# Kernel tuning notes

Hardware: AMD Instinct MI355X
Metric: run time of the kernel (lower is better)

Reference implementation:

```python
import jax, jax.numpy as jnp
import numpy as np

B, S, D = 2, 2048, 640
H, DH = 8, 80  # heads, dim_head
SCALE = DH ** -0.5


def setup_inputs() -> dict:
    key = jax.random.key(0)
    ks = jax.random.split(key, 7)
    std = D ** -0.5
    return {
        "x": jax.random.normal(ks[0], (B, S, D), jnp.float32),
        "encoder_hidden_states": jax.random.normal(ks[1], (B, S, D), jnp.float32),
        # Linear weights stored as [in, out] so application is x @ W
        "Wq": jax.random.normal(ks[2], (D, H * DH), jnp.float32) * std,
        "Wk": jax.random.normal(ks[3], (D, H * DH), jnp.float32) * std,
        "Wv": jax.random.normal(ks[4], (D, H * DH), jnp.float32) * std,
        "Wo": jax.random.normal(ks[5], (H * DH, D), jnp.float32) * std,
        "bo": jax.random.normal(ks[6], (D,), jnp.float32) * 0.01,
    }


def reference(x, encoder_hidden_states, Wq, Wk, Wv, Wo, bo):
    # projections (to_q/to_k/to_v have bias=False)
    q = x @ Wq                      # [B, S, H*DH]
    k = encoder_hidden_states @ Wk  # [B, S, H*DH]
    v = encoder_hidden_states @ Wv  # [B, S, H*DH]

    def split_heads(t):
        b, s, _ = t.shape
        return t.reshape(b, s, H, DH).transpose(0, 2, 1, 3)  # [B, H, S, DH]

    q, k, v = split_heads(q), split_heads(k), split_heads(v)

    # the torch loop over bh-chunks computes plain softmax attention; same math fused
    scores = jnp.einsum("bhid,bhjd->bhij", q, k) * SCALE  # [B, H, Sq, Skv]
    attn = jax.nn.softmax(scores, axis=-1)
    out = jnp.einsum("bhij,bhjd->bhid", attn, v)          # [B, H, Sq, DH]

    out = out.transpose(0, 2, 1, 3).reshape(x.shape[0], x.shape[1], H * DH)
    return out @ Wo + bo  # to_out[0]; Dropout(p=0) is identity
```

## Files before the change

### kernel.cpp

```cpp
#include <hip/hip_runtime.h>
#include <hip/hip_bf16.h>

typedef __bf16 v4bf __attribute__((ext_vector_type(4)));
typedef __bf16 v8bf __attribute__((ext_vector_type(8)));
typedef float  v4f  __attribute__((ext_vector_type(4)));

namespace {
constexpr int Bb  = 2;
constexpr int Ss  = 2048;
constexpr int Dd  = 640;
constexpr int Hh  = 8;
constexpr int DHh = 80;
constexpr int Mm  = Bb * Ss;
constexpr float kQScale = 0.11180339887498949f * 1.4426950408889634f;

__device__ __forceinline__ float4 ld4(const float* p) {
  return *reinterpret_cast<const float4*>(p);
}
}

__global__ __launch_bounds__(256)
void wtrans_kernel(const float* __restrict__ Wq, const float* __restrict__ Wk,
                   const float* __restrict__ Wv, const float* __restrict__ Wo,
                   __bf16* __restrict__ Wtq, __bf16* __restrict__ Wtk,
                   __bf16* __restrict__ Wtv, __bf16* __restrict__ Wto) {
  const int z = blockIdx.z;
  const float* W = (z == 0) ? Wq : (z == 1) ? Wk : (z == 2) ? Wv : Wo;
  __bf16* Wt = (z == 0) ? Wtq : (z == 1) ? Wtk : (z == 2) ? Wtv : Wto;
  const int k0 = blockIdx.y * 32, n0 = blockIdx.x * 32;
  __shared__ float t[32][33];
  const int tid = threadIdx.x;
  {
    int kr = tid >> 3, c4 = (tid & 7) * 4;
    float4 f = ld4(W + (size_t)(k0 + kr) * Dd + n0 + c4);
    t[kr][c4 + 0] = f.x; t[kr][c4 + 1] = f.y;
    t[kr][c4 + 2] = f.z; t[kr][c4 + 3] = f.w;
  }
  __syncthreads();
  {
    int nr = tid >> 3, kc = (tid & 7) * 4;
    v4bf p;
#pragma unroll
    for (int u = 0; u < 4; ++u) p[u] = (__bf16)t[kc + u][nr];
    *reinterpret_cast<v4bf*>(&Wt[(size_t)(n0 + nr) * Dd + k0 + kc]) = p;
  }
}

template <bool AF32>
__device__ __forceinline__ void gemm_core_db(const void* __restrict__ Ap,
                                             const __bf16* __restrict__ Bt,
                                             __bf16* As, __bf16* Bs, int m0,
                                             int n0, int rh, int ch,
                                             v4f acc[4][4]) {
  constexpr int BUF = 128 * 40;
  constexpr int NKB = Dd / 32;
  const int tid = threadIdx.x;
  const int lane = tid & 63;
  const int quad = lane >> 4, l15 = lane & 15;
  const int lr = tid >> 1;
  const int lk = (tid & 1) * 16;
  const __bf16* Bg = Bt + (size_t)(n0 + lr) * Dd + lk;
  const float* Af = (const float*)Ap;
  const __bf16* Ab = (const __bf16*)Ap;

#pragma unroll
  for (int i = 0; i < 4; ++i)
#pragma unroll
    for (int j = 0; j < 4; ++j) acc[i][j] = (v4f){0.f, 0.f, 0.f, 0.f};

  v8bf a0, a1, b0, b1;
  if constexpr (AF32) {
    const float* ap = Af + (size_t)(m0 + lr) * Dd + lk;
    float4 f0 = ld4(ap), f1 = ld4(ap + 4), f2 = ld4(ap + 8), f3 = ld4(ap + 12);
    a0[0]=(__bf16)f0.x; a0[1]=(__bf16)f0.y; a0[2]=(__bf16)f0.z; a0[3]=(__bf16)f0.w;
    a0[4]=(__bf16)f1.x; a0[5]=(__bf16)f1.y; a0[6]=(__bf16)f1.z; a0[7]=(__bf16)f1.w;
    a1[0]=(__bf16)f2.x; a1[1]=(__bf16)f2.y; a1[2]=(__bf16)f2.z; a1[3]=(__bf16)f2.w;
    a1[4]=(__bf16)f3.x; a1[5]=(__bf16)f3.y; a1[6]=(__bf16)f3.z; a1[7]=(__bf16)f3.w;
  } else {
    const __bf16* ap = Ab + (size_t)(m0 + lr) * Dd + lk;
    a0 = *reinterpret_cast<const v8bf*>(ap);
    a1 = *reinterpret_cast<const v8bf*>(ap + 8);
  }
  b0 = *reinterpret_cast<const v8bf*>(Bg);
  b1 = *reinterpret_cast<const v8bf*>(Bg + 8);
  *reinterpret_cast<v8bf*>(&As[lr * 40 + lk])     = a0;
  *reinterpret_cast<v8bf*>(&As[lr * 40 + lk + 8]) = a1;
  *reinterpret_cast<v8bf*>(&Bs[lr * 40 + lk])     = b0;
  *reinterpret_cast<v8bf*>(&Bs[lr * 40 + lk + 8]) = b1;

  for (int it = 0; it < NKB; ++it) {
    if (it + 1 < NKB) {
      const int kb = (it + 1) * 32;
      if constexpr (AF32) {
        const float* ap = Af + (size_t)(m0 + lr) * Dd + kb + lk;
        float4 f0 = ld4(ap), f1 = ld4(ap + 4), f2 = ld4(ap + 8),
               f3 = ld4(ap + 12);
        a0[0]=(__bf16)f0.x; a0[1]=(__bf16)f0.y; a0[2]=(__bf16)f0.z; a0[3]=(__bf16)f0.w;
        a0[4]=(__bf16)f1.x; a0[5]=(__bf16)f1.y; a0[6]=(__bf16)f1.z; a0[7]=(__bf16)f1.w;
        a1[0]=(__bf16)f2.x; a1[1]=(__bf16)f2.y; a1[2]=(__bf16)f2.z; a1[3]=(__bf16)f2.w;
        a1[4]=(__bf16)f3.x; a1[5]=(__bf16)f3.y; a1[6]=(__bf16)f3.z; a1[7]=(__bf16)f3.w;
      } else {
        const __bf16* ap = Ab + (size_t)(m0 + lr) * Dd + kb + lk;
        a0 = *reinterpret_cast<const v8bf*>(ap);
        a1 = *reinterpret_cast<const v8bf*>(ap + 8);
      }
      b0 = *reinterpret_cast<const v8bf*>(Bg + kb);
      b1 = *reinterpret_cast<const v8bf*>(Bg + kb + 8);
    }
    __syncthreads();
    const int cur = (it & 1) * BUF, nxt = BUF - cur;
    v8bf af[4], bv[4];
#pragma unroll
    for (int i = 0; i < 4; ++i)
      af[i] = *reinterpret_cast<const v8bf*>(
          &As[cur + (rh + i * 16 + l15) * 40 + quad * 8]);
#pragma unroll
    for (int j = 0; j < 4; ++j)
      bv[j] = *reinterpret_cast<const v8bf*>(
          &Bs[cur + (ch + j * 16 + l15) * 40 + quad * 8]);
#pragma unroll
    for (int i = 0; i < 4; ++i)
#pragma unroll
      for (int j = 0; j < 4; ++j)
        acc[i][j] = __builtin_amdgcn_mfma_f32_16x16x32_bf16(af[i], bv[j],
                                                            acc[i][j], 0, 0, 0);
    if (it + 1 < NKB) {
      *reinterpret_cast<v8bf*>(&As[nxt + lr * 40 + lk])     = a0;
      *reinterpret_cast<v8bf*>(&As[nxt + lr * 40 + lk + 8]) = a1;
      *reinterpret_cast<v8bf*>(&Bs[nxt + lr * 40 + lk])     = b0;
      *reinterpret_cast<v8bf*>(&Bs[nxt + lr * 40 + lk + 8]) = b1;
    }
  }
}

__global__ __launch_bounds__(256)
void gemm_qkv_mfma(const float* __restrict__ x, const float* __restrict__ ehs,
                   const __bf16* __restrict__ Wtq,
                   const __bf16* __restrict__ Wtk,
                   const __bf16* __restrict__ Wtv, __bf16* __restrict__ qb,
                   __bf16* __restrict__ kbuf, __bf16* __restrict__ vb) {
  const int z = blockIdx.z;
  const float* A = (z == 0) ? x : ehs;
  const __bf16* Bt = (z == 0) ? Wtq : (z == 1) ? Wtk : Wtv;
  __bf16* C = (z == 0) ? qb : (z == 1) ? kbuf : vb;
  const float scale = (z == 0) ? kQScale : 1.0f;

  __shared__ __bf16 As[2 * 128 * 40];
  __shared__ __bf16 Bs[2 * 128 * 40];
  const int tid = threadIdx.x;
  const int w = tid >> 6, lane = tid & 63;
  const int quad = lane >> 4, l15 = lane & 15;
  const int m0 = blockIdx.y * 128, n0 = blockIdx.x * 128;
  const int rh = (w >> 1) * 64, ch = (w & 1) * 64;
  v4f acc[4][4];
  gemm_core_db<true>(A, Bt, As, Bs, m0, n0, rh, ch, acc);

  if (z == 2) {
#pragma unroll
    for (int i = 0; i < 4; ++i)
#pragma unroll
      for (int j = 0; j < 4; ++j) {
        int m = m0 + rh + i * 16 + quad * 4;
        int n = n0 + ch + j * 16 + l15;
        int bb = m >> 11, tok = m & 2047;
        v4bf pk;
#pragma unroll
        for (int r = 0; r < 4; ++r) pk[r] = (__bf16)acc[i][j][r];
        *reinterpret_cast<v4bf*>(&C[((size_t)bb * Dd + n) * Ss + tok]) = pk;
      }
  } else {
#pragma unroll
    for (int i = 0; i < 4; ++i)
#pragma unroll
      for (int j = 0; j < 4; ++j) {
        int m = m0 + rh + i * 16 + quad * 4;
        int n = n0 + ch + j * 16 + l15;
        int hh = n / DHh, d = n % DHh;
        int bb = m >> 11, tok = m & 2047;
        __bf16* base = &C[(((size_t)bb * Hh + hh) * Ss + tok) * DHh + d];
#pragma unroll
        for (int r = 0; r < 4; ++r)
          base[(size_t)r * DHh] = (__bf16)(acc[i][j][r] * scale);
      }
  }
}

__global__ __launch_bounds__(256)
void gemm_out_mfma(const __bf16* __restrict__ A, const __bf16* __restrict__ Bt,
                   const float* __restrict__ bias, float* __restrict__ out) {
  __shared__ __bf16 As[2 * 128 * 40];
  __shared__ __bf16 Bs[2 * 128 * 40];
  const int tid = threadIdx.x;
  const int w = tid >> 6, lane = tid & 63;
  const int quad = lane >> 4, l15 = lane & 15;
  const int m0 = blockIdx.y * 128, n0 = blockIdx.x * 128;
  const int rh = (w >> 1) * 64, ch = (w & 1) * 64;
  v4f acc[4][4];
  gemm_core_db<false>(A, Bt, As, Bs, m0, n0, rh, ch, acc);

#pragma unroll
  for (int i = 0; i < 4; ++i)
#pragma unroll
    for (int j = 0; j < 4; ++j) {
      int m = m0 + rh + i * 16 + quad * 4;
      int n = n0 + ch + j * 16 + l15;
      float bn = bias[n];
#pragma unroll
      for (int r = 0; r < 4; ++r)
        out[(size_t)(m + r) * Dd + n] = acc[i][j][r] + bn;
    }
}

__global__ __launch_bounds__(256, 2)
void attn_mfma_kernel(const __bf16* __restrict__ q,
                      const __bf16* __restrict__ k,
                      const __bf16* __restrict__ vtg, __bf16* __restrict__ o) {
  constexpr int QT = 64;
  constexpr int KT = 32;
  constexpr int KW = Ss / 4;
  constexpr int NIT = KW / KT;
  constexpr int LQ = 104;
  constexpr int LV = 40;
  constexpr int KS = KT * LQ;
  constexpr int VS = 96 * LV;
  constexpr int PS = QT * LV;
  constexpr int WSZ = KS + VS + PS;
  constexpr int LM = 100;

  __shared__ __align__(16) __bf16 smem[4 * WSZ];

  const int bh = blockIdx.x;
  const int b = bh >> 3, h = bh & 7;
  const int q0 = blockIdx.y * QT;
  const int tid = threadIdx.x;
  const int w = tid >> 6;
  const int lane = tid & 63;
  const int quad = lane >> 4;
  const int l15 = lane & 15;

  __bf16* ksw = smem + w * WSZ;
  __bf16* vtw = ksw + KS;
  __bf16* psw = vtw + VS;

  const __bf16* qg  = q + ((size_t)(b * Hh + h) * Ss + q0) * DHh;
  const __bf16* kgb = k + (size_t)(b * Hh + h) * Ss * DHh;
  const __bf16* vgb = vtg + ((size_t)b * Dd + h * DHh) * Ss;

  v8bf qf[4][3];
#pragma unroll
  for (int qt = 0; qt < 4; ++qt)
#pragma unroll
    for (int s = 0; s < 3; ++s) {
      if (s == 2 && quad >= 2) {
        qf[qt][s] = (v8bf){};
      } else {
        qf[qt][s] = *reinterpret_cast<const v8bf*>(
            qg + (size_t)(qt * 16 + l15) * DHh + s * 32 + quad * 8);
      }
    }

  int klr[5];
#pragma unroll
  for (int c = 0; c < 5; ++c) {
    int E = c * 512 + lane * 8;
    klr[c] = (E / DHh) * LQ + (E % DHh);
  }
  const int vgo = (lane >> 2) * Ss + (lane & 3) * 8;
  const int vlo = (lane >> 2) * LV + (lane & 3) * 8;

  {
    v8bf z8 = {};
    *reinterpret_cast<v8bf*>(&ksw[(lane >> 1) * LQ + 80 + (lane & 1) * 8]) = z8;
    v8bf pad = {};
    int vr = 80 + (lane >> 2);
    if (vr == 80) {
#pragma unroll
      for (int e = 0; e < 8; ++e) pad[e] = (__bf16)1.f;
    }
    *reinterpret_cast<v8bf*>(&vtw[vr * LV + (lane & 3) * 8]) = pad;
  }
  {
    const __bf16* kg = kgb + (size_t)(w * KW) * DHh;
#pragma unroll
    for (int c = 0; c < 5; ++c)
      *reinterpret_cast<v8bf*>(&ksw[klr[c]]) =
          *reinterpret_cast<const v8bf*>(kg + c * 512 + lane * 8);
  }

  v4f Oacc[4][6];
#pragma unroll
  for (int qt = 0; qt < 4; ++qt)
#pragma unroll
    for (int mt = 0; mt < 6; ++mt) Oacc[qt][mt] = (v4f){0.f, 0.f, 0.f, 0.f};

  for (int it = 0; it < NIT; ++it) {
    const bool pfK = (it + 1 < NIT);
    v8bf kreg[5];
    if (pfK) {
      const __bf16* kg = kgb + (size_t)(w * KW + (it + 1) * KT) * DHh;
#pragma unroll
      for (int c = 0; c < 5; ++c)
        kreg[c] = *reinterpret_cast<const v8bf*>(kg + c * 512 + lane * 8);
    }

    v4f sacc[4][2];
#pragma unroll
    for (int qt = 0; qt < 4; ++qt) {
      sacc[qt][0] = (v4f){0.f, 0.f, 0.f, 0.f};
      sacc[qt][1] = (v4f){0.f, 0.f, 0.f, 0.f};
    }
    __builtin_amdgcn_s_setprio(1);
#pragma unroll
    for (int s = 0; s < 3; ++s) {
      v8bf ak0 = *reinterpret_cast<const v8bf*>(
          &ksw[l15 * LQ + s * 32 + quad * 8]);
      v8bf ak1 = *reinterpret_cast<const v8bf*>(
          &ksw[(16 + l15) * LQ + s * 32 + quad * 8]);
#pragma unroll
      for (int qt = 0; qt < 4; ++qt) {
        sacc[qt][0] = __builtin_amdgcn_mfma_f32_16x16x32_bf16(
            ak0, qf[qt][s], sacc[qt][0], 0, 0, 0);
        sacc[qt][1] = __builtin_amdgcn_mfma_f32_16x16x32_bf16(
            ak1, qf[qt][s], sacc[qt][1], 0, 0, 0);
      }
    }

    v8bf vreg[5];
    {
      const __bf16* vg = vgb + (w * KW + it * KT);
#pragma unroll
      for (int c = 0; c < 5; ++c)
        vreg[c] = *reinterpret_cast<const v8bf*>(vg + vgo +
                                                 (size_t)c * 16 * Ss);
    }

    if (it > 0) {
      v8bf bp[4];
#pragma unroll
      for (int qt = 0; qt < 4; ++qt)
        bp[qt] = *reinterpret_cast<const v8bf*>(
            &psw[(qt * 16 + l15) * LV + quad * 8]);
#pragma unroll
      for (int mt = 0; mt < 6; ++mt) {
        v8bf av = *reinterpret_cast<const v8bf*>(
            &vtw[(mt * 16 + l15) * LV + quad * 8]);
#pragma unroll
        for (int qt = 0; qt < 4; ++qt)
          Oacc[qt][mt] = __builtin_amdgcn_mfma_f32_16x16x32_bf16(
              av, bp[qt], Oacc[qt][mt], 0, 0, 0);
      }
    }
    __builtin_amdgcn_s_setprio(0);

#pragma unroll
    for (int qt = 0; qt < 4; ++qt)
#pragma unroll
      for (int mt = 0; mt < 2; ++mt) {
        v4bf pk;
#pragma unroll
        for (int r = 0; r < 4; ++r) pk[r] = (__bf16)exp2f(sacc[qt][mt][r]);
        *reinterpret_cast<v4bf*>(
            &psw[(qt * 16 + l15) * LV + mt * 16 + quad * 4]) = pk;
      }

    if (pfK) {
#pragma unroll
      for (int c = 0; c < 5; ++c)
        *reinterpret_cast<v8bf*>(&ksw[klr[c]]) = kreg[c];
    }
#pragma unroll
    for (int c = 0; c < 5; ++c)
      *reinterpret_cast<v8bf*>(&vtw[vlo + c * 16 * LV]) = vreg[c];
  }

  {
    v8bf bp[4];
#pragma unroll
    for (int qt = 0; qt < 4; ++qt)
      bp[qt] = *reinterpret_cast<const v8bf*>(
          &psw[(qt * 16 + l15) * LV + quad * 8]);
    __builtin_amdgcn_s_setprio(1);
#pragma unroll
    for (int mt = 0; mt < 6; ++mt) {
      v8bf av = *reinterpret_cast<const v8bf*>(
          &vtw[(mt * 16 + l15) * LV + quad * 8]);
#pragma unroll
      for (int qt = 0; qt < 4; ++qt)
        Oacc[qt][mt] = __builtin_amdgcn_mfma_f32_16x16x32_bf16(
            av, bp[qt], Oacc[qt][mt], 0, 0, 0);
    }
    __builtin_amdgcn_s_setprio(0);
  }

  __syncthreads();
  float* mrg = (float*)smem;
  if (w >= 2) {
    float* base = mrg + (w - 2) * (QT * LM);
#pragma unroll
    for (int qt = 0; qt < 4; ++qt)
#pragma unroll
      for (int mt = 0; mt < 6; ++mt)
        *reinterpret_cast<v4f*>(
            &base[(qt * 16 + l15) * LM + mt * 16 + quad * 4]) = Oacc[qt][mt];
  }
  __syncthreads();
  if (w < 2) {
    const float* base = mrg + w * (QT * LM);
#pragma unroll
    for (int qt = 0; qt < 4; ++qt)
#pragma unroll
      for (int mt = 0; mt < 6; ++mt)
        Oacc[qt][mt] += *reinterpret_cast<const v4f*>(
            &base[(qt * 16 + l15) * LM + mt * 16 + quad * 4]);
  }
  __syncthreads();
  if (w == 1) {
#pragma unroll
    for (int qt = 0; qt < 4; ++qt)
#pragma unroll
      for (int mt = 0; mt < 6; ++mt)
        *reinterpret_cast<v4f*>(
            &mrg[(qt * 16 + l15) * LM + mt * 16 + quad * 4]) = Oacc[qt][mt];
  }
  __syncthreads();
  if (w == 0) {
#pragma unroll
    for (int qt = 0; qt < 4; ++qt)
#pragma unroll
      for (int mt = 0; mt < 6; ++mt)
        Oacc[qt][mt] += *reinterpret_cast<const v4f*>(
            &mrg[(qt * 16 + l15) * LM + mt * 16 + quad * 4]);
#pragma unroll
    for (int qt = 0; qt < 4; ++qt) {
      float lsum = __shfl(Oacc[qt][5][0], l15);
      float inv = 1.f / lsum;
      __bf16* og =
          o + (size_t)(b * Ss + q0 + qt * 16 + l15) * Dd + h * DHh;
#pragma unroll
      for (int mt = 0; mt < 5; ++mt) {
        v4bf pk;
#pragma unroll
        for (int r = 0; r < 4; ++r) pk[r] = (__bf16)(Oacc[qt][mt][r] * inv);
        *reinterpret_cast<v4bf*>(&og[mt * 16 + quad * 4]) = pk;
      }
    }
  }
}

extern "C" void kernel_launch(void* const* d_in, const int* in_sizes, int n_in,
                              void* d_out, int out_size, void* d_ws,
                              size_t ws_size, hipStream_t stream) {
  const float* x   = (const float*)d_in[0];
  const float* ehs = (const float*)d_in[1];
  const float* Wq  = (const float*)d_in[2];
  const float* Wk  = (const float*)d_in[3];
  const float* Wv  = (const float*)d_in[4];
  const float* Wo  = (const float*)d_in[5];
  const float* bo  = (const float*)d_in[6];
  float* out = (float*)d_out;

  __bf16* qb  = (__bf16*)d_ws;
  __bf16* kb  = qb + (size_t)Mm * Dd;
  __bf16* vb  = kb + (size_t)Mm * Dd;
  __bf16* ab  = vb + (size_t)Mm * Dd;
  __bf16* Wtq = ab + (size_t)Mm * Dd;
  __bf16* Wtk = Wtq + (size_t)Dd * Dd;
  __bf16* Wtv = Wtk + (size_t)Dd * Dd;
  __bf16* Wto = Wtv + (size_t)Dd * Dd;

  wtrans_kernel<<<dim3(Dd / 32, Dd / 32, 4), 256, 0, stream>>>(
      Wq, Wk, Wv, Wo, Wtq, Wtk, Wtv, Wto);
  gemm_qkv_mfma<<<dim3(Dd / 128, Mm / 128, 3), 256, 0, stream>>>(
      x, ehs, Wtq, Wtk, Wtv, qb, kb, vb);
  attn_mfma_kernel<<<dim3(Bb * Hh, Ss / 64), 256, 0, stream>>>(qb, kb, vb, ab);
  gemm_out_mfma<<<dim3(Dd / 128, Mm / 128), 256, 0, stream>>>(ab, Wto, bo,
                                                              out);
}
```

Measured before the change: 155.8 us.

## Fuse K and V projections sharing one A tile; use raw v_exp_f32 in attention

The QKV GEMM now launches two block types per output tile. One computes Q from x, the other computes both K and V from encoder_hidden_states. The second reuses a single loaded and bf16-converted A tile for two B matrices, which avoids reading and converting ehs twice. It doubles the accumulator registers (launch_bounds with 1 block), adds a third LDS buffer, and makes the two block types unbalanced in work. The attention softmax also replaces exp2f with the raw v_exp_f32 instruction, which skips the denormal and range handling.

```diff
diff --git a/kernel.cpp b/kernel.cpp
--- a/kernel.cpp
+++ b/kernel.cpp
@@ -16,6 +16,19 @@
 
 __device__ __forceinline__ float4 ld4(const float* p) {
   return *reinterpret_cast<const float4*>(p);
+}
+
+__device__ __forceinline__ v8bf pack8(float4 f0, float4 f1) {
+  v8bf p;
+  p[0]=(__bf16)f0.x; p[1]=(__bf16)f0.y; p[2]=(__bf16)f0.z; p[3]=(__bf16)f0.w;
+  p[4]=(__bf16)f1.x; p[5]=(__bf16)f1.y; p[6]=(__bf16)f1.z; p[7]=(__bf16)f1.w;
+  return p;
+}
+
+__device__ __forceinline__ float exp2_hw(float x) {
+  float r;
+  asm("v_exp_f32 %0, %1" : "=v"(r) : "v"(x));
+  return r;
 }
 }
 
@@ -71,11 +84,8 @@
   v8bf a0, a1, b0, b1;
   if constexpr (AF32) {
     const float* ap = Af + (size_t)(m0 + lr) * Dd + lk;
-    float4 f0 = ld4(ap), f1 = ld4(ap + 4), f2 = ld4(ap + 8), f3 = ld4(ap + 12);
-    a0[0]=(__bf16)f0.x; a0[1]=(__bf16)f0.y; a0[2]=(__bf16)f0.z; a0[3]=(__bf16)f0.w;
-    a0[4]=(__bf16)f1.x; a0[5]=(__bf16)f1.y; a0[6]=(__bf16)f1.z; a0[7]=(__bf16)f1.w;
-    a1[0]=(__bf16)f2.x; a1[1]=(__bf16)f2.y; a1[2]=(__bf16)f2.z; a1[3]=(__bf16)f2.w;
-    a1[4]=(__bf16)f3.x; a1[5]=(__bf16)f3.y; a1[6]=(__bf16)f3.z; a1[7]=(__bf16)f3.w;
+    a0 = pack8(ld4(ap), ld4(ap + 4));
+    a1 = pack8(ld4(ap + 8), ld4(ap + 12));
   } else {
     const __bf16* ap = Ab + (size_t)(m0 + lr) * Dd + lk;
     a0 = *reinterpret_cast<const v8bf*>(ap);
@@ -93,12 +103,8 @@
       const int kb = (it + 1) * 32;
       if constexpr (AF32) {
         const float* ap = Af + (size_t)(m0 + lr) * Dd + kb + lk;
-        float4 f0 = ld4(ap), f1 = ld4(ap + 4), f2 = ld4(ap + 8),
-               f3 = ld4(ap + 12);
-        a0[0]=(__bf16)f0.x; a0[1]=(__bf16)f0.y; a0[2]=(__bf16)f0.z; a0[3]=(__bf16)f0.w;
-        a0[4]=(__bf16)f1.x; a0[5]=(__bf16)f1.y; a0[6]=(__bf16)f1.z; a0[7]=(__bf16)f1.w;
-        a1[0]=(__bf16)f2.x; a1[1]=(__bf16)f2.y; a1[2]=(__bf16)f2.z; a1[3]=(__bf16)f2.w;
-        a1[4]=(__bf16)f3.x; a1[5]=(__bf16)f3.y; a1[6]=(__bf16)f3.z; a1[7]=(__bf16)f3.w;
+        a0 = pack8(ld4(ap), ld4(ap + 4));
+        a1 = pack8(ld4(ap + 8), ld4(ap + 12));
       } else {
         const __bf16* ap = Ab + (size_t)(m0 + lr) * Dd + kb + lk;
         a0 = *reinterpret_cast<const v8bf*>(ap);
@@ -133,29 +139,139 @@
   }
 }
 
-__global__ __launch_bounds__(256)
+__global__ __launch_bounds__(256, 1)
 void gemm_qkv_mfma(const float* __restrict__ x, const float* __restrict__ ehs,
                    const __bf16* __restrict__ Wtq,
                    const __bf16* __restrict__ Wtk,
                    const __bf16* __restrict__ Wtv, __bf16* __restrict__ qb,
                    __bf16* __restrict__ kbuf, __bf16* __restrict__ vb) {
-  const int z = blockIdx.z;
-  const float* A = (z == 0) ? x : ehs;
-  const __bf16* Bt = (z == 0) ? Wtq : (z == 1) ? Wtk : Wtv;
-  __bf16* C = (z == 0) ? qb : (z == 1) ? kbuf : vb;
-  const float scale = (z == 0) ? kQScale : 1.0f;
-
-  __shared__ __bf16 As[2 * 128 * 40];
-  __shared__ __bf16 Bs[2 * 128 * 40];
+  constexpr int BUF = 128 * 40;
+  constexpr int NKB = Dd / 32;
+  const int z = blockIdx.x;
+  __shared__ __bf16 As[2 * BUF];
+  __shared__ __bf16 B0s[2 * BUF];
+  __shared__ __bf16 B1s[2 * BUF];
   const int tid = threadIdx.x;
   const int w = tid >> 6, lane = tid & 63;
   const int quad = lane >> 4, l15 = lane & 15;
-  const int m0 = blockIdx.y * 128, n0 = blockIdx.x * 128;
+  const int m0 = blockIdx.z * 128, n0 = blockIdx.y * 128;
   const int rh = (w >> 1) * 64, ch = (w & 1) * 64;
-  v4f acc[4][4];
-  gemm_core_db<true>(A, Bt, As, Bs, m0, n0, rh, ch, acc);
-
-  if (z == 2) {
+  const int lr = tid >> 1, lk = (tid & 1) * 16;
+
+  const float* A = z ? ehs : x;
+  const __bf16* Bt0 = z ? Wtk : Wtq;
+  const float* Ag = A + (size_t)(m0 + lr) * Dd + lk;
+  const __bf16* B0g = Bt0 + (size_t)(n0 + lr) * Dd + lk;
+  const __bf16* B1g = Wtv + (size_t)(n0 + lr) * Dd + lk;
+
+  v4f acc0[4][4], acc1[4][4];
+#pragma unroll
+  for (int i = 0; i < 4; ++i)
+#pragma unroll
+    for (int j = 0; j < 4; ++j) {
+      acc0[i][j] = (v4f){0.f, 0.f, 0.f, 0.f};
+      acc1[i][j] = (v4f){0.f, 0.f, 0.f, 0.f};
+    }
+
+  v8bf a0, a1, b00, b01, b10, b11;
+  a0 = pack8(ld4(Ag), ld4(Ag + 4));
+  a1 = pack8(ld4(Ag + 8), ld4(Ag + 12));
+  b00 = *reinterpret_cast<const v8bf*>(B0g);
+  b01 = *reinterpret_cast<const v8bf*>(B0g + 8);
+  if (z) {
+    b10 = *reinterpret_cast<const v8bf*>(B1g);
+    b11 = *reinterpret_cast<const v8bf*>(B1g + 8);
+  }
+  *reinterpret_cast<v8bf*>(&As[lr * 40 + lk])      = a0;
+  *reinterpret_cast<v8bf*>(&As[lr * 40 + lk + 8])  = a1;
+  *reinterpret_cast<v8bf*>(&B0s[lr * 40 + lk])     = b00;
+  *reinterpret_cast<v8bf*>(&B0s[lr * 40 + lk + 8]) = b01;
+  if (z) {
+    *reinterpret_cast<v8bf*>(&B1s[lr * 40 + lk])     = b10;
+    *reinterpret_cast<v8bf*>(&B1s[lr * 40 + lk + 8]) = b11;
+  }
+
+  for (int it = 0; it < NKB; ++it) {
+    if (it + 1 < NKB) {
+      const int kb = (it + 1) * 32;
+      a0 = pack8(ld4(Ag + kb), ld4(Ag + kb + 4));
+      a1 = pack8(ld4(Ag + kb + 8), ld4(Ag + kb + 12));
+      b00 = *reinterpret_cast<const v8bf*>(B0g + kb);
+      b01 = *reinterpret_cast<const v8bf*>(B0g + kb + 8);
+      if (z) {
+        b10 = *reinterpret_cast<const v8bf*>(B1g + kb);
+        b11 = *reinterpret_cast<const v8bf*>(B1g + kb + 8);
+      }
+    }
+    __syncthreads();
+    const int cur = (it & 1) * BUF, nxt = BUF - cur;
+    v8bf af[4], bv[4];
+#pragma unroll
+    for (int i = 0; i < 4; ++i)
+      af[i] = *reinterpret_cast<const v8bf*>(
+          &As[cur + (rh + i * 16 + l15) * 40 + quad * 8]);
+#pragma unroll
+    for (int j = 0; j < 4; ++j)
+      bv[j] = *reinterpret_cast<const v8bf*>(
+          &B0s[cur + (ch + j * 16 + l15) * 40 + quad * 8]);
+#pragma unroll
+    for (int i = 0; i < 4; ++i)
+#pragma unroll
+      for (int j = 0; j < 4; ++j)
+        acc0[i][j] = __builtin_amdgcn_mfma_f32_16x16x32_bf16(
+            af[i], bv[j], acc0[i][j], 0, 0, 0);
+    if (z) {
+#pragma unroll
+      for (int j = 0; j < 4; ++j)
+        bv[j] = *reinterpret_cast<const v8bf*>(
+            &B1s[cur + (ch + j * 16 + l15) * 40 + quad * 8]);
+#pragma unroll
+      for (int i = 0; i < 4; ++i)
+#pragma unroll
+        for (int j = 0; j < 4; ++j)
+          acc1[i][j] = __builtin_amdgcn_mfma_f32_16x16x32_bf16(
+              af[i], bv[j], acc1[i][j], 0, 0, 0);
+    }
+    if (it + 1 < NKB) {
+      *reinterpret_cast<v8bf*>(&As[nxt + lr * 40 + lk])      = a0;
+      *reinterpret_cast<v8bf*>(&As[nxt + lr * 40 + lk + 8])  = a1;
+      *reinterpret_cast<v8bf*>(&B0s[nxt + lr * 40 + lk])     = b00;
+      *reinterpret_cast<v8bf*>(&B0s[nxt + lr * 40 + lk + 8]) = b01;
+      if (z) {
+        *reinterpret_cast<v8bf*>(&B1s[nxt + lr * 40 + lk])     = b10;
+        *reinterpret_cast<v8bf*>(&B1s[nxt + lr * 40 + lk + 8]) = b11;
+      }
+    }
+  }
+
+  if (z == 0) {
+#pragma unroll
+    for (int i = 0; i < 4; ++i)
+#pragma unroll
+      for (int j = 0; j < 4; ++j) {
+        int m = m0 + rh + i * 16 + quad * 4;
+        int n = n0 + ch + j * 16 + l15;
+        int hh = n / DHh, d = n % DHh;
+        int bb = m >> 11, tok = m & 2047;
+        __bf16* base = &qb[(((size_t)bb * Hh + hh) * Ss + tok) * DHh + d];
+#pragma unroll
+        for (int r = 0; r < 4; ++r)
+          base[(size_t)r * DHh] = (__bf16)(acc0[i][j][r] * kQScale);
+      }
+  } else {
+#pragma unroll
+    for (int i = 0; i < 4; ++i)
+#pragma unroll
+      for (int j = 0; j < 4; ++j) {
+        int m = m0 + rh + i * 16 + quad * 4;
+        int n = n0 + ch + j * 16 + l15;
+        int hh = n / DHh, d = n % DHh;
+        int bb = m >> 11, tok = m & 2047;
+        __bf16* base = &kbuf[(((size_t)bb * Hh + hh) * Ss + tok) * DHh + d];
+#pragma unroll
+        for (int r = 0; r < 4; ++r)
+          base[(size_t)r * DHh] = (__bf16)acc0[i][j][r];
+      }
 #pragma unroll
     for (int i = 0; i < 4; ++i)
 #pragma unroll
@@ -165,22 +281,8 @@
         int bb = m >> 11, tok = m & 2047;
         v4bf pk;
 #pragma unroll
-        for (int r = 0; r < 4; ++r) pk[r] = (__bf16)acc[i][j][r];
-        *reinterpret_cast<v4bf*>(&C[((size_t)bb * Dd + n) * Ss + tok]) = pk;
-      }
-  } else {
-#pragma unroll
-    for (int i = 0; i < 4; ++i)
-#pragma unroll
-      for (int j = 0; j < 4; ++j) {
-        int m = m0 + rh + i * 16 + quad * 4;
-        int n = n0 + ch + j * 16 + l15;
-        int hh = n / DHh, d = n % DHh;
-        int bb = m >> 11, tok = m & 2047;
-        __bf16* base = &C[(((size_t)bb * Hh + hh) * Ss + tok) * DHh + d];
-#pragma unroll
-        for (int r = 0; r < 4; ++r)
-          base[(size_t)r * DHh] = (__bf16)(acc[i][j][r] * scale);
+        for (int r = 0; r < 4; ++r) pk[r] = (__bf16)acc1[i][j][r];
+        *reinterpret_cast<v4bf*>(&vb[((size_t)bb * Dd + n) * Ss + tok]) = pk;
       }
   }
 }
@@ -358,7 +460,8 @@
       for (int mt = 0; mt < 2; ++mt) {
         v4bf pk;
 #pragma unroll
-        for (int r = 0; r < 4; ++r) pk[r] = (__bf16)exp2f(sacc[qt][mt][r]);
+        for (int r = 0; r < 4; ++r)
+          pk[r] = (__bf16)exp2_hw(sacc[qt][mt][r]);
         *reinterpret_cast<v4bf*>(
             &psw[(qt * 16 + l15) * LV + mt * 16 + quad * 4]) = pk;
       }
@@ -470,7 +573,7 @@
 
   wtrans_kernel<<<dim3(Dd / 32, Dd / 32, 4), 256, 0, stream>>>(
       Wq, Wk, Wv, Wo, Wtq, Wtk, Wtv, Wto);
-  gemm_qkv_mfma<<<dim3(Dd / 128, Mm / 128, 3), 256, 0, stream>>>(
+  gemm_qkv_mfma<<<dim3(2, Dd / 128, Mm / 128), 256, 0, stream>>>(
       x, ehs, Wtq, Wtk, Wtv, qb, kb, vb);
   attn_mfma_kernel<<<dim3(Bb * Hh, Ss / 64), 256, 0, stream>>>(qb, kb, vb, ab);
   gemm_out_mfma<<<dim3(Dd / 128, Mm / 128), 256, 0, stream>>>(ab, Wto, bo,
```

New measurement: 174.7 us. +12.2%, slower.
